# Kernel optimization log

Measured on AMD Instinct MI355X. Metric: run time of the kernel, lower is better.

Reference implementation:

```python
import jax, jax.numpy as jnp
import numpy as np

N_NODES = 100000
N_REL = 8
N_EDGES = 1_600_000
ED = 64   # entity_dim
RD = 64   # relation_dim
H = 4     # attention heads
A = 16    # attention dim per head
D1, D2 = 32, 16  # conv_dim_list


def _leaky(x):
    return jax.nn.leaky_relu(x, 0.01)  # nn.LeakyReLU default slope


def _l2norm(x):
    n = jnp.sqrt(jnp.sum(x * x, axis=1, keepdims=True))
    return x / jnp.maximum(n, 1e-12)  # F.normalize(p=2, dim=1)


def setup_inputs() -> dict:
    key = jax.random.key(0)
    ks = jax.random.split(key, 16)
    s = 0.1
    return dict(
        src=jax.random.randint(ks[0], (N_EDGES,), 0, N_NODES),
        dst=jax.random.randint(ks[1], (N_EDGES,), 0, N_NODES),
        etype=jax.random.randint(ks[2], (N_EDGES,), 0, N_REL),
        node_ids=jnp.arange(N_NODES),
        user_ids=jax.random.randint(ks[3], (1000,), 0, N_NODES),
        item_ids=jax.random.randint(ks[4], (4096,), 0, N_NODES),
        entity_embed=jax.random.normal(ks[5], (N_NODES, ED)) * s,
        rel_embed=jax.random.normal(ks[6], (N_REL, RD)) * s,
        W_R=jax.random.normal(ks[7], (N_REL, ED, RD)) * s,
        W_A=jax.random.normal(ks[8], (RD, H, A)) * s,
        W1_0=jax.random.normal(ks[9], (ED, D1 // H)) * s,
        b1_0=jnp.zeros((D1 // H,)),
        W2_0=jax.random.normal(ks[10], (ED, D1 // H)) * s,
        b2_0=jnp.zeros((D1 // H,)),
        W1_1=jax.random.normal(ks[11], (D1, D2 // H)) * s,
        b1_1=jnp.zeros((D2 // H,)),
        W2_1=jax.random.normal(ks[12], (D1, D2 // H)) * s,
        b2_1=jnp.zeros((D2 // H,)),
    )


def _compute_attention(entity_embed, rel_embed, W_R, W_A, src, dst, etype):
    # relation-specific edge attention: tanh(e_src W_r W_A) * tanh(e_dst W_r W_A + r W_A)
    WA_flat = W_A.reshape(RD, H * A)
    W_ra = jnp.einsum('rij,jk->rik', W_R, WA_flat)          # [R, ED, H*A]
    proj = jnp.einsum('ne,rek->rnk', entity_embed, W_ra)    # [R, N, H*A]
    r_emb_a = rel_embed @ WA_flat                           # [R, H*A]
    r_mul_t = jnp.tanh(proj[etype, src])                    # [E, H*A]
    r_mul_h = jnp.tanh(proj[etype, dst] + r_emb_a[etype])   # [E, H*A]
    att = (r_mul_t * r_mul_h).reshape(-1, H, A).sum(-1)     # [E, H]
    # edge softmax over incoming edges of each dst node, per head
    m = jax.ops.segment_max(att, dst, num_segments=N_NODES)
    m = jnp.where(jnp.isfinite(m), m, 0.0)
    e = jnp.exp(att - m[dst])
    z = jax.ops.segment_sum(e, dst, num_segments=N_NODES)
    return e / jnp.maximum(z[dst], 1e-12)                   # [E, H]


def _bi_layer(ego, att, src, dst, W1, b1, W2, b2, out_dim):
    # u_mul_e + sum: message = node[src] (broadcast over heads) * att[:, :, None]
    in_dim = ego.shape[1]
    msg = ego[src][:, None, :] * att[:, :, None]            # [E, H, in]
    N_h = jax.ops.segment_sum(msg, dst, num_segments=N_NODES)  # [N, H, in]
    node = ego[:, None, :]                                  # [N, 1, in]
    out1 = _leaky((node + N_h).reshape(-1, in_dim) @ W1 + b1).reshape(N_NODES, out_dim)
    out2 = _leaky((node * N_h).reshape(-1, in_dim) @ W2 + b2).reshape(N_NODES, out_dim)
    return out1 + out2  # dropout p=0 (eval)


def reference(src, dst, etype, node_ids, user_ids, item_ids,
              entity_embed, rel_embed, W_R, W_A,
              W1_0, b1_0, W2_0, b2_0, W1_1, b1_1, W2_1, b2_1):
    att = _compute_attention(entity_embed, rel_embed, W_R, W_A, src, dst, etype)
    ego = entity_embed[node_ids]
    ego1 = _bi_layer(ego, att, src, dst, W1_0, b1_0, W2_0, b2_0, D1)
    ego2 = _bi_layer(ego1, att, src, dst, W1_1, b1_1, W2_1, b2_1, D2)
    all_embed = jnp.concatenate([ego, _l2norm(ego1), _l2norm(ego2)], axis=1)  # [N, 112]
    return all_embed[user_ids] @ all_embed[item_ids].T     # [1000, 4096]
```

## Files before the change

### kernel.cpp

```cpp
#include <hip/hip_runtime.h>
#include <hip/hip_bf16.h>
#include <math.h>

#define NN 100000
#define NR 8
#define NE 1600000

typedef __attribute__((ext_vector_type(8))) short short8v;
typedef __attribute__((ext_vector_type(4))) float float4v;
typedef __attribute__((ext_vector_type(2))) float float2v;

__device__ inline float bf2f(unsigned short u) {
  union { unsigned int i; float f; } v; v.i = ((unsigned int)u) << 16; return v.f;
}
__device__ inline unsigned short f2bf(float f) {
  __hip_bfloat16 h = __float2bfloat16(f);
  return *reinterpret_cast<unsigned short*>(&h);
}
__device__ inline float fast_tanh(float x) {
  float ex = __expf(2.f * x);
  return 1.f - 2.f * __builtin_amdgcn_rcpf(ex + 1.f);
}

__global__ void k_prep(const float* __restrict__ W_R, const float* __restrict__ W_A,
                       const float* __restrict__ rel, unsigned short* __restrict__ Wbf,
                       float* __restrict__ r_emb_a) {
  int tid = blockIdx.x * 256 + threadIdx.x;
  if (tid < NR * 64 * 64) {
    int r = tid >> 12;
    int i = (tid >> 6) & 63;
    int k = tid & 63;
    float acc = 0.f;
    const float* wr = W_R + (r * 64 + i) * 64;
    for (int j = 0; j < 64; ++j) acc += wr[j] * W_A[j * 64 + k];
    Wbf[(r * 64 + k) * 64 + i] = f2bf(acc);
  } else if (tid < NR * 64 * 64 + NR * 64) {
    int idx = tid - NR * 64 * 64;
    int r = idx >> 6, k = idx & 63;
    float acc = 0.f;
    for (int j = 0; j < 64; ++j) acc += rel[r * 64 + j] * W_A[j * 64 + k];
    r_emb_a[idx] = acc;
  }
}

__global__ void k_cvt(const float* __restrict__ E, unsigned short* __restrict__ Ebf) {
  int i = blockIdx.x * 256 + threadIdx.x;
  float4 v = ((const float4*)E)[i];
  ushort4 o;
  o.x = f2bf(v.x); o.y = f2bf(v.y); o.z = f2bf(v.z); o.w = f2bf(v.w);
  ((ushort4*)Ebf)[i] = o;
}

__global__ void k_proj(const unsigned short* __restrict__ Ebf,
                       const unsigned short* __restrict__ Wbf,
                       const float* __restrict__ rea,
                       unsigned char* __restrict__ T1n, unsigned char* __restrict__ T2n) {
  int wv = threadIdx.x >> 6, lane = threadIdx.x & 63;
  int n0 = blockIdx.x * 64 + wv * 16;
  int mrow = lane & 15, kg = lane >> 4;
  int node = n0 + mrow;
  int nodeC = (node < NN) ? node : NN - 1;
  bool ok = (node < NN);
  const short8v b0 = *(const short8v*)(Ebf + (long)nodeC * 64 + kg * 8);
  const short8v b1 = *(const short8v*)(Ebf + (long)nodeC * 64 + 32 + kg * 8);
  for (int ct = 0; ct < 32; ++ct) {
    int ca = ct * 16 + mrow;
    const short8v a0 = *(const short8v*)(Wbf + ca * 64 + kg * 8);
    const short8v a1 = *(const short8v*)(Wbf + ca * 64 + 32 + kg * 8);
    float4v acc = {0.f, 0.f, 0.f, 0.f};
    acc = __builtin_amdgcn_mfma_f32_16x16x32_bf16(a0, b0, acc, 0, 0, 0);
    acc = __builtin_amdgcn_mfma_f32_16x16x32_bf16(a1, b1, acc, 0, 0, 0);
    int c0 = ct * 16 + kg * 4;
    float4 rv4 = *(const float4*)(rea + c0);
    unsigned int p1 = __builtin_amdgcn_cvt_pk_fp8_f32(fast_tanh(acc[0]), fast_tanh(acc[1]), 0u, false);
    p1 = __builtin_amdgcn_cvt_pk_fp8_f32(fast_tanh(acc[2]), fast_tanh(acc[3]), p1, true);
    unsigned int p2 = __builtin_amdgcn_cvt_pk_fp8_f32(fast_tanh(acc[0] + rv4.x), fast_tanh(acc[1] + rv4.y), 0u, false);
    p2 = __builtin_amdgcn_cvt_pk_fp8_f32(fast_tanh(acc[2] + rv4.z), fast_tanh(acc[3] + rv4.w), p2, true);
    if (ok) {
      *(unsigned int*)(T1n + (long)node * 512 + c0) = p1;
      *(unsigned int*)(T2n + (long)node * 512 + c0) = p2;
    }
  }
}

__global__ void k_hist(const int* __restrict__ dst, int* __restrict__ cnt) {
  int e = blockIdx.x * 256 + threadIdx.x;
  if (e < NE) atomicAdd(&cnt[dst[e]], 1);
}

#define SCAN_B 1024
#define NSCAN ((NN + SCAN_B - 1) / SCAN_B)

__global__ void k_scan1(const int* __restrict__ cnt, int* __restrict__ rowp,
                        int* __restrict__ bsum) {
  __shared__ int s[SCAN_B];
  int t = threadIdx.x, g = blockIdx.x * SCAN_B + t;
  s[t] = (g < NN) ? cnt[g] : 0;
  __syncthreads();
  for (int off = 1; off < SCAN_B; off <<= 1) {
    int x = (t >= off) ? s[t - off] : 0;
    __syncthreads();
    s[t] += x;
    __syncthreads();
  }
  if (g < NN) rowp[g + 1] = s[t];
  if (t == SCAN_B - 1) bsum[blockIdx.x] = s[t];
}

__global__ void k_scan2(int* bsum) {
  if (threadIdx.x == 0) {
    int acc = 0;
    for (int i = 0; i < NSCAN; ++i) { int v = bsum[i]; bsum[i] = acc; acc += v; }
  }
}

__global__ void k_scan3(int* rowp, const int* __restrict__ bsum) {
  int t = threadIdx.x, g = blockIdx.x * SCAN_B + t;
  if (g < NN) rowp[g + 1] += bsum[blockIdx.x];
  if (g == 0) rowp[0] = 0;
}

__global__ void k_scatter(const int* __restrict__ src, const int* __restrict__ dst,
                          const int* __restrict__ etype, const int* __restrict__ rowp,
                          int* __restrict__ cur, uint2* __restrict__ rec) {
  int e = blockIdx.x * 256 + threadIdx.x;
  if (e >= NE) return;
  int d = dst[e];
  int p = rowp[d] + atomicAdd(&cur[d], 1);
  uint2 rv;
  rv.x = ((unsigned int)src[e] << 3) | (unsigned int)etype[e];
  rv.y = (unsigned int)d;
  rec[p] = rv;
}

__global__ void k_att(const unsigned char* __restrict__ T1n,
                      const unsigned char* __restrict__ T2n,
                      const uint2* __restrict__ rec, int* __restrict__ srcs,
                      float* __restrict__ att) {
  int gid = blockIdx.x * 256 + threadIdx.x;
  int e = gid >> 2;
  int h = gid & 3;
  if (e >= NE) return;
  uint2 rv = rec[e];
  int r = rv.x & 7;
  int s = rv.x >> 3;
  int d = (int)rv.y;
  const uint4 av = *(const uint4*)(T1n + (long)s * 512 + r * 64 + h * 16);
  const uint4 bv = *(const uint4*)(T2n + (long)d * 512 + r * 64 + h * 16);
  const unsigned int* ap = (const unsigned int*)&av;
  const unsigned int* bp = (const unsigned int*)&bv;
  float acc = 0.f;
#pragma unroll
  for (int i = 0; i < 4; ++i) {
    float2v a0 = __builtin_amdgcn_cvt_pk_f32_fp8(ap[i], false);
    float2v a1 = __builtin_amdgcn_cvt_pk_f32_fp8(ap[i], true);
    float2v b0 = __builtin_amdgcn_cvt_pk_f32_fp8(bp[i], false);
    float2v b1 = __builtin_amdgcn_cvt_pk_f32_fp8(bp[i], true);
    acc += a0.x * b0.x + a0.y * b0.y + a1.x * b1.x + a1.y * b1.y;
  }
  att[gid] = acc;
  if (h == 0) srcs[e] = s;
}

__global__ void k_nodemax(const int* __restrict__ rowp, const float* __restrict__ att,
                          float* __restrict__ minv) {
  int gid = blockIdx.x * 256 + threadIdx.x;
  int n = gid >> 2, h = gid & 3;
  if (n >= NN) return;
  int p0 = rowp[n], p1 = rowp[n + 1];
  float m = -3.4e38f;
  for (int p = p0; p < p1; ++p) m = fmaxf(m, att[p * 4 + h]);
  float z = 0.f;
  for (int p = p0; p < p1; ++p) z += __expf(att[p * 4 + h] - m);
  minv[n * 8 + h] = m;
  minv[n * 8 + 4 + h] = 1.f / fmaxf(z, 1e-12f);
}

__global__ void k_fused0(const float* __restrict__ E, const unsigned short* __restrict__ Ebf,
                         const float* __restrict__ att, const float* __restrict__ minv,
                         const int* __restrict__ rowp, const int* __restrict__ srcs,
                         const float* __restrict__ W1, const float* __restrict__ b1,
                         const float* __restrict__ W2, const float* __restrict__ b2,
                         float* __restrict__ ego1, unsigned short* __restrict__ ego1bf) {
  __shared__ float wt1[8][68], wt2[8][68];
  __shared__ float bb[16];
  __shared__ float s1[4][4][68], s2[4][4][68];
  int t = threadIdx.x;
  for (int i = t; i < 512; i += 256) {
    int d = i >> 3, j = i & 7;
    wt1[j][d] = W1[i];
    wt2[j][d] = W2[i];
  }
  if (t < 8) bb[t] = b1[t];
  else if (t < 16) bb[t] = b2[t - 8];
  __syncthreads();
  int wv = t >> 6, lane = t & 63;
  int n = blockIdx.x * 4 + wv;
  int p0 = rowp[n], p1 = rowp[n + 1];
  int g = lane >> 4, q = lane & 15;
  float4 mh = *(const float4*)(minv + n * 8);
  float4 zh = *(const float4*)(minv + n * 8 + 4);
  float acc[4][4];
#pragma unroll
  for (int h = 0; h < 4; ++h)
#pragma unroll
    for (int j = 0; j < 4; ++j) acc[h][j] = 0.f;
  for (int p = p0 + g; p < p1; p += 4) {
    int s = srcs[p];
    float4 a = ((const float4*)att)[p];
    a.x = __expf(a.x - mh.x) * zh.x;
    a.y = __expf(a.y - mh.y) * zh.y;
    a.z = __expf(a.z - mh.z) * zh.z;
    a.w = __expf(a.w - mh.w) * zh.w;
    ushort4 ev = *(const ushort4*)(Ebf + s * 64 + q * 4);
    float e0 = bf2f(ev.x), e1 = bf2f(ev.y), e2 = bf2f(ev.z), e3 = bf2f(ev.w);
    acc[0][0] += a.x * e0; acc[0][1] += a.x * e1; acc[0][2] += a.x * e2; acc[0][3] += a.x * e3;
    acc[1][0] += a.y * e0; acc[1][1] += a.y * e1; acc[1][2] += a.y * e2; acc[1][3] += a.y * e3;
    acc[2][0] += a.z * e0; acc[2][1] += a.z * e1; acc[2][2] += a.z * e2; acc[2][3] += a.z * e3;
    acc[3][0] += a.w * e0; acc[3][1] += a.w * e1; acc[3][2] += a.w * e2; acc[3][3] += a.w * e3;
  }
#pragma unroll
  for (int h = 0; h < 4; ++h)
#pragma unroll
    for (int j = 0; j < 4; ++j) {
      acc[h][j] += __shfl_xor(acc[h][j], 16);
      acc[h][j] += __shfl_xor(acc[h][j], 32);
    }
  if (lane < 16) {
    float4 edv = *(const float4*)(E + n * 64 + q * 4);
#pragma unroll
    for (int h = 0; h < 4; ++h) {
      float4 v1, v2;
      v1.x = edv.x + acc[h][0]; v2.x = edv.x * acc[h][0];
      v1.y = edv.y + acc[h][1]; v2.y = edv.y * acc[h][1];
      v1.z = edv.z + acc[h][2]; v2.z = edv.z * acc[h][2];
      v1.w = edv.w + acc[h][3]; v2.w = edv.w * acc[h][3];
      *(float4*)&s1[wv][h][q * 4] = v1;
      *(float4*)&s2[wv][h][q * 4] = v2;
    }
  }
  __syncthreads();
  int h = (lane >> 3) & 3, j = lane & 7;
  const float* sp = (lane < 32) ? &s1[wv][h][0] : &s2[wv][h][0];
  const float* wp = (lane < 32) ? &wt1[j][0] : &wt2[j][0];
  float o = 0.f;
#pragma unroll
  for (int d = 0; d < 64; d += 4) {
    float4 sv = *(const float4*)(sp + d);
    float4 wv4 = *(const float4*)(wp + d);
    o += sv.x * wv4.x + sv.y * wv4.y + sv.z * wv4.z + sv.w * wv4.w;
  }
  o += (lane < 32) ? bb[j] : bb[8 + j];
  o = (o >= 0.f) ? o : 0.01f * o;
  float other = __shfl_xor(o, 32);
  if (lane < 32) {
    float r = o + other;
    ego1[n * 32 + h * 8 + j] = r;
    ego1bf[n * 32 + h * 8 + j] = f2bf(r);
  }
}

__global__ void k_fused1(const float* __restrict__ ego1, const unsigned short* __restrict__ E1bf,
                         const float* __restrict__ att, const float* __restrict__ minv,
                         const int* __restrict__ rowp, const int* __restrict__ srcs,
                         const float* __restrict__ W1, const float* __restrict__ b1,
                         const float* __restrict__ W2, const float* __restrict__ b2,
                         float* __restrict__ ego2) {
  __shared__ float wt1[4][36], wt2[4][36], bb[8];
  __shared__ float s1[4][4][36], s2[4][4][36];
  int t = threadIdx.x;
  if (t < 128) { int d = t >> 2, j = t & 3; wt1[j][d] = W1[t]; wt2[j][d] = W2[t]; }
  if (t < 4) bb[t] = b1[t];
  else if (t < 8) bb[t] = b2[t - 4];
  __syncthreads();
  int wv = t >> 6, lane = t & 63;
  int n = blockIdx.x * 4 + wv;
  int p0 = rowp[n], p1 = rowp[n + 1];
  int g = lane >> 3, q = lane & 7;
  float4 mh = *(const float4*)(minv + n * 8);
  float4 zh = *(const float4*)(minv + n * 8 + 4);
  float acc[4][4];
#pragma unroll
  for (int h = 0; h < 4; ++h)
#pragma unroll
    for (int j = 0; j < 4; ++j) acc[h][j] = 0.f;
  for (int p = p0 + g; p < p1; p += 8) {
    int s = srcs[p];
    float4 a = ((const float4*)att)[p];
    a.x = __expf(a.x - mh.x) * zh.x;
    a.y = __expf(a.y - mh.y) * zh.y;
    a.z = __expf(a.z - mh.z) * zh.z;
    a.w = __expf(a.w - mh.w) * zh.w;
    ushort4 ev = *(const ushort4*)(E1bf + s * 32 + q * 4);
    float e0 = bf2f(ev.x), e1 = bf2f(ev.y), e2 = bf2f(ev.z), e3 = bf2f(ev.w);
    acc[0][0] += a.x * e0; acc[0][1] += a.x * e1; acc[0][2] += a.x * e2; acc[0][3] += a.x * e3;
    acc[1][0] += a.y * e0; acc[1][1] += a.y * e1; acc[1][2] += a.y * e2; acc[1][3] += a.y * e3;
    acc[2][0] += a.z * e0; acc[2][1] += a.z * e1; acc[2][2] += a.z * e2; acc[2][3] += a.z * e3;
    acc[3][0] += a.w * e0; acc[3][1] += a.w * e1; acc[3][2] += a.w * e2; acc[3][3] += a.w * e3;
  }
#pragma unroll
  for (int h = 0; h < 4; ++h)
#pragma unroll
    for (int j = 0; j < 4; ++j) {
      acc[h][j] += __shfl_xor(acc[h][j], 8);
      acc[h][j] += __shfl_xor(acc[h][j], 16);
      acc[h][j] += __shfl_xor(acc[h][j], 32);
    }
  if (lane < 8) {
    float4 e1v = *(const float4*)(ego1 + n * 32 + q * 4);
#pragma unroll
    for (int h = 0; h < 4; ++h) {
      float4 v1, v2;
      v1.x = e1v.x + acc[h][0]; v2.x = e1v.x * acc[h][0];
      v1.y = e1v.y + acc[h][1]; v2.y = e1v.y * acc[h][1];
      v1.z = e1v.z + acc[h][2]; v2.z = e1v.z * acc[h][2];
      v1.w = e1v.w + acc[h][3]; v2.w = e1v.w * acc[h][3];
      *(float4*)&s1[wv][h][q * 4] = v1;
      *(float4*)&s2[wv][h][q * 4] = v2;
    }
  }
  __syncthreads();
  if (lane < 32) {
    int h = (lane >> 2) & 3, j = lane & 3;
    const float* sp = (lane < 16) ? &s1[wv][h][0] : &s2[wv][h][0];
    const float* wp = (lane < 16) ? &wt1[j][0] : &wt2[j][0];
    float o = 0.f;
#pragma unroll
    for (int d = 0; d < 32; d += 4) {
      float4 sv = *(const float4*)(sp + d);
      float4 wv4 = *(const float4*)(wp + d);
      o += sv.x * wv4.x + sv.y * wv4.y + sv.z * wv4.z + sv.w * wv4.w;
    }
    o += (lane < 16) ? bb[j] : bb[4 + j];
    o = (o >= 0.f) ? o : 0.01f * o;
    float other = __shfl_xor(o, 16);
    if (lane < 16) ego2[n * 16 + h * 4 + j] = o + other;
  }
}

__global__ void k_uv(const float* __restrict__ E, const float* __restrict__ E1,
                     const float* __restrict__ E2, const int* __restrict__ uid,
                     const int* __restrict__ iid, float* __restrict__ U,
                     float* __restrict__ V) {
  int row = (blockIdx.x * 256 + threadIdx.x) >> 6;
  int lane = threadIdx.x & 63;
  if (row >= 1000 + 4096) return;
  int id = (row < 1000) ? uid[row] : iid[row - 1000];
  float* dest = (row < 1000) ? (U + row * 112) : (V + (row - 1000) * 112);
  float v1 = (lane < 32) ? E1[id * 32 + lane] : 0.f;
  float s1 = v1 * v1;
  for (int m = 1; m < 64; m <<= 1) s1 += __shfl_xor(s1, m);
  float v2 = (lane < 16) ? E2[id * 16 + lane] : 0.f;
  float s2 = v2 * v2;
  for (int m = 1; m < 64; m <<= 1) s2 += __shfl_xor(s2, m);
  float i1 = 1.f / fmaxf(sqrtf(s1), 1e-12f);
  float i2 = 1.f / fmaxf(sqrtf(s2), 1e-12f);
  dest[lane] = E[id * 64 + lane];
  if (lane < 32) dest[64 + lane] = v1 * i1;
  if (lane < 16) dest[96 + lane] = v2 * i2;
}

__global__ void k_gemm(const float* __restrict__ U, const float* __restrict__ V,
                       float* __restrict__ C) {
  __shared__ float Us[16][113], Vs[16][113];
  int tx = threadIdx.x & 15, ty = threadIdx.x >> 4;
  int u0 = blockIdx.y * 16, v0 = blockIdx.x * 16;
  for (int i = threadIdx.x; i < 16 * 112; i += 256) {
    int rr = i / 112, cc = i % 112;
    int ur = u0 + rr;
    Us[rr][cc] = (ur < 1000) ? U[ur * 112 + cc] : 0.f;
    Vs[rr][cc] = V[(v0 + rr) * 112 + cc];
  }
  __syncthreads();
  int u = u0 + ty;
  if (u >= 1000) return;
  float acc = 0.f;
#pragma unroll
  for (int k = 0; k < 112; ++k) acc += Us[ty][k] * Vs[tx][k];
  C[u * 4096 + v0 + tx] = acc;
}

extern "C" void kernel_launch(void* const* d_in, const int* in_sizes, int n_in,
                              void* d_out, int out_size, void* d_ws, size_t ws_size,
                              hipStream_t stream) {
  const int* src = (const int*)d_in[0];
  const int* dst = (const int*)d_in[1];
  const int* etype = (const int*)d_in[2];
  const int* uid = (const int*)d_in[4];
  const int* iid = (const int*)d_in[5];
  const float* entity = (const float*)d_in[6];
  const float* rel = (const float*)d_in[7];
  const float* W_R = (const float*)d_in[8];
  const float* W_A = (const float*)d_in[9];
  const float* W1_0 = (const float*)d_in[10];
  const float* b1_0 = (const float*)d_in[11];
  const float* W2_0 = (const float*)d_in[12];
  const float* b2_0 = (const float*)d_in[13];
  const float* W1_1 = (const float*)d_in[14];
  const float* b1_1 = (const float*)d_in[15];
  const float* W2_1 = (const float*)d_in[16];
  const float* b2_1 = (const float*)d_in[17];
  float* out = (float*)d_out;

  char* ws = (char*)d_ws;
  unsigned char*  T1n  = (unsigned char*) (ws + 0);
  float*          ego1 = (float*)         (ws + 0);
  unsigned short* e1bf = (unsigned short*)(ws + 12800000);
  float*          ego2 = (float*)         (ws + 19200000);
  float*          U    = (float*)         (ws + 25600000);
  float*          V    = (float*)         (ws + 26048000);
  unsigned char*  T2n  = (unsigned char*) (ws + 51200000);
  float*          att  = (float*)         (ws + 102400000);
  uint2*          rec  = (uint2*)         (ws + 128000000);
  int*            srcs = (int*)           (ws + 140800000);
  int*            rowp = (int*)           (ws + 147200000);
  int*            cnt  = (int*)           (ws + 147600128);
  int*            bsum = (int*)           (ws + 148000256);
  unsigned short* Wbf  = (unsigned short*)(ws + 148000768);
  float*          rea  = (float*)         (ws + 148066304);
  unsigned short* Ebf  = (unsigned short*)(ws + 148068352);
  float*          minv = (float*)         (ws + 160868352);

  hipMemsetAsync(cnt, 0, NN * sizeof(int), stream);
  k_prep<<<130, 256, 0, stream>>>(W_R, W_A, rel, Wbf, rea);
  k_cvt<<<6250, 256, 0, stream>>>(entity, Ebf);
  k_proj<<<(NN + 63) / 64, 256, 0, stream>>>(Ebf, Wbf, rea, T1n, T2n);
  k_hist<<<NE / 256, 256, 0, stream>>>(dst, cnt);
  k_scan1<<<NSCAN, SCAN_B, 0, stream>>>(cnt, rowp, bsum);
  k_scan2<<<1, 64, 0, stream>>>(bsum);
  k_scan3<<<NSCAN, SCAN_B, 0, stream>>>(rowp, bsum);
  hipMemsetAsync(cnt, 0, NN * sizeof(int), stream);
  k_scatter<<<NE / 256, 256, 0, stream>>>(src, dst, etype, rowp, cnt, rec);
  k_att<<<NE * 4 / 256, 256, 0, stream>>>(T1n, T2n, rec, srcs, att);
  k_nodemax<<<(NN * 4 + 255) / 256, 256, 0, stream>>>(rowp, att, minv);
  k_fused0<<<NN / 4, 256, 0, stream>>>(entity, Ebf, att, minv, rowp, srcs,
                                       W1_0, b1_0, W2_0, b2_0, ego1, e1bf);
  k_fused1<<<NN / 4, 256, 0, stream>>>(ego1, e1bf, att, minv, rowp, srcs,
                                       W1_1, b1_1, W2_1, b2_1, ego2);
  k_uv<<<(1000 + 4096 + 3) / 4, 256, 0, stream>>>(entity, ego1, ego2, uid, iid, U, V);
  k_gemm<<<dim3(4096 / 16, (1000 + 15) / 16), 256, 0, stream>>>(U, V, out);
}
```

Baseline: 594.8 us.

## Fuse edge attention and softmax normalization into layer-0 aggregation kernel

Computes edge attention dot products inside the per-destination-node aggregation kernel, drops the separate attention and segment-max/sum kernels, and skips the max subtraction since attention values are bounded. Unnormalized exp weights are accumulated and the sum reciprocal is applied at the end; exp weights and inverse sums are stored for the second layer. This removes two launches and the round trips for att, srcs and min/inv stats, at the cost of extra shuffles per edge inside the fused loop and reliance on bounded logits for numerical safety.

```diff
diff --git a/kernel.cpp b/kernel.cpp
--- a/kernel.cpp
+++ b/kernel.cpp
@@ -133,52 +133,11 @@
   rec[p] = rv;
 }
 
-__global__ void k_att(const unsigned char* __restrict__ T1n,
-                      const unsigned char* __restrict__ T2n,
-                      const uint2* __restrict__ rec, int* __restrict__ srcs,
-                      float* __restrict__ att) {
-  int gid = blockIdx.x * 256 + threadIdx.x;
-  int e = gid >> 2;
-  int h = gid & 3;
-  if (e >= NE) return;
-  uint2 rv = rec[e];
-  int r = rv.x & 7;
-  int s = rv.x >> 3;
-  int d = (int)rv.y;
-  const uint4 av = *(const uint4*)(T1n + (long)s * 512 + r * 64 + h * 16);
-  const uint4 bv = *(const uint4*)(T2n + (long)d * 512 + r * 64 + h * 16);
-  const unsigned int* ap = (const unsigned int*)&av;
-  const unsigned int* bp = (const unsigned int*)&bv;
-  float acc = 0.f;
-#pragma unroll
-  for (int i = 0; i < 4; ++i) {
-    float2v a0 = __builtin_amdgcn_cvt_pk_f32_fp8(ap[i], false);
-    float2v a1 = __builtin_amdgcn_cvt_pk_f32_fp8(ap[i], true);
-    float2v b0 = __builtin_amdgcn_cvt_pk_f32_fp8(bp[i], false);
-    float2v b1 = __builtin_amdgcn_cvt_pk_f32_fp8(bp[i], true);
-    acc += a0.x * b0.x + a0.y * b0.y + a1.x * b1.x + a1.y * b1.y;
-  }
-  att[gid] = acc;
-  if (h == 0) srcs[e] = s;
-}
-
-__global__ void k_nodemax(const int* __restrict__ rowp, const float* __restrict__ att,
-                          float* __restrict__ minv) {
-  int gid = blockIdx.x * 256 + threadIdx.x;
-  int n = gid >> 2, h = gid & 3;
-  if (n >= NN) return;
-  int p0 = rowp[n], p1 = rowp[n + 1];
-  float m = -3.4e38f;
-  for (int p = p0; p < p1; ++p) m = fmaxf(m, att[p * 4 + h]);
-  float z = 0.f;
-  for (int p = p0; p < p1; ++p) z += __expf(att[p * 4 + h] - m);
-  minv[n * 8 + h] = m;
-  minv[n * 8 + 4 + h] = 1.f / fmaxf(z, 1e-12f);
-}
-
 __global__ void k_fused0(const float* __restrict__ E, const unsigned short* __restrict__ Ebf,
-                         const float* __restrict__ att, const float* __restrict__ minv,
-                         const int* __restrict__ rowp, const int* __restrict__ srcs,
+                         const unsigned char* __restrict__ T1n,
+                         const unsigned char* __restrict__ T2n,
+                         const uint2* __restrict__ rec, const int* __restrict__ rowp,
+                         float* __restrict__ att4, float* __restrict__ zinv4,
                          const float* __restrict__ W1, const float* __restrict__ b1,
                          const float* __restrict__ W2, const float* __restrict__ b2,
                          float* __restrict__ ego1, unsigned short* __restrict__ ego1bf) {
@@ -198,26 +157,39 @@
   int n = blockIdx.x * 4 + wv;
   int p0 = rowp[n], p1 = rowp[n + 1];
   int g = lane >> 4, q = lane & 15;
-  float4 mh = *(const float4*)(minv + n * 8);
-  float4 zh = *(const float4*)(minv + n * 8 + 4);
+  int bl = (lane & 48) | (lane & 3);
+  const unsigned int* recw = (const unsigned int*)rec;
   float acc[4][4];
 #pragma unroll
   for (int h = 0; h < 4; ++h)
 #pragma unroll
     for (int j = 0; j < 4; ++j) acc[h][j] = 0.f;
+  float z0 = 0.f, z1 = 0.f, z2 = 0.f, z3 = 0.f;
   for (int p = p0 + g; p < p1; p += 4) {
-    int s = srcs[p];
-    float4 a = ((const float4*)att)[p];
-    a.x = __expf(a.x - mh.x) * zh.x;
-    a.y = __expf(a.y - mh.y) * zh.y;
-    a.z = __expf(a.z - mh.z) * zh.z;
-    a.w = __expf(a.w - mh.w) * zh.w;
+    unsigned int rv = recw[p * 2];
+    int s = (int)(rv >> 3), r = (int)(rv & 7);
+    unsigned int aw = *(const unsigned int*)(T1n + (long)s * 512 + r * 64 + q * 4);
+    unsigned int bw = *(const unsigned int*)(T2n + (long)n * 512 + r * 64 + q * 4);
+    float2v fa0 = __builtin_amdgcn_cvt_pk_f32_fp8(aw, false);
+    float2v fa1 = __builtin_amdgcn_cvt_pk_f32_fp8(aw, true);
+    float2v fb0 = __builtin_amdgcn_cvt_pk_f32_fp8(bw, false);
+    float2v fb1 = __builtin_amdgcn_cvt_pk_f32_fp8(bw, true);
+    float dot = fa0.x * fb0.x + fa0.y * fb0.y + fa1.x * fb1.x + fa1.y * fb1.y;
+    dot += __shfl_xor(dot, 1);
+    dot += __shfl_xor(dot, 2);
+    float e = __expf(dot);
+    float e0 = __shfl(e, bl);
+    float e1 = __shfl(e, bl + 4);
+    float e2 = __shfl(e, bl + 8);
+    float e3 = __shfl(e, bl + 12);
+    z0 += e0; z1 += e1; z2 += e2; z3 += e3;
+    if (q == 0) ((float4*)att4)[p] = make_float4(e0, e1, e2, e3);
     ushort4 ev = *(const ushort4*)(Ebf + s * 64 + q * 4);
-    float e0 = bf2f(ev.x), e1 = bf2f(ev.y), e2 = bf2f(ev.z), e3 = bf2f(ev.w);
-    acc[0][0] += a.x * e0; acc[0][1] += a.x * e1; acc[0][2] += a.x * e2; acc[0][3] += a.x * e3;
-    acc[1][0] += a.y * e0; acc[1][1] += a.y * e1; acc[1][2] += a.y * e2; acc[1][3] += a.y * e3;
-    acc[2][0] += a.z * e0; acc[2][1] += a.z * e1; acc[2][2] += a.z * e2; acc[2][3] += a.z * e3;
-    acc[3][0] += a.w * e0; acc[3][1] += a.w * e1; acc[3][2] += a.w * e2; acc[3][3] += a.w * e3;
+    float v0 = bf2f(ev.x), v1 = bf2f(ev.y), v2 = bf2f(ev.z), v3 = bf2f(ev.w);
+    acc[0][0] += e0 * v0; acc[0][1] += e0 * v1; acc[0][2] += e0 * v2; acc[0][3] += e0 * v3;
+    acc[1][0] += e1 * v0; acc[1][1] += e1 * v1; acc[1][2] += e1 * v2; acc[1][3] += e1 * v3;
+    acc[2][0] += e2 * v0; acc[2][1] += e2 * v1; acc[2][2] += e2 * v2; acc[2][3] += e2 * v3;
+    acc[3][0] += e3 * v0; acc[3][1] += e3 * v1; acc[3][2] += e3 * v2; acc[3][3] += e3 * v3;
   }
 #pragma unroll
   for (int h = 0; h < 4; ++h)
@@ -226,17 +198,30 @@
       acc[h][j] += __shfl_xor(acc[h][j], 16);
       acc[h][j] += __shfl_xor(acc[h][j], 32);
     }
+  z0 += __shfl_xor(z0, 16); z0 += __shfl_xor(z0, 32);
+  z1 += __shfl_xor(z1, 16); z1 += __shfl_xor(z1, 32);
+  z2 += __shfl_xor(z2, 16); z2 += __shfl_xor(z2, 32);
+  z3 += __shfl_xor(z3, 16); z3 += __shfl_xor(z3, 32);
+  float zi0 = 1.f / fmaxf(z0, 1e-12f);
+  float zi1 = 1.f / fmaxf(z1, 1e-12f);
+  float zi2 = 1.f / fmaxf(z2, 1e-12f);
+  float zi3 = 1.f / fmaxf(z3, 1e-12f);
+  if (lane == 0) *(float4*)(zinv4 + n * 4) = make_float4(zi0, zi1, zi2, zi3);
   if (lane < 16) {
+    acc[0][0] *= zi0; acc[0][1] *= zi0; acc[0][2] *= zi0; acc[0][3] *= zi0;
+    acc[1][0] *= zi1; acc[1][1] *= zi1; acc[1][2] *= zi1; acc[1][3] *= zi1;
+    acc[2][0] *= zi2; acc[2][1] *= zi2; acc[2][2] *= zi2; acc[2][3] *= zi2;
+    acc[3][0] *= zi3; acc[3][1] *= zi3; acc[3][2] *= zi3; acc[3][3] *= zi3;
     float4 edv = *(const float4*)(E + n * 64 + q * 4);
 #pragma unroll
     for (int h = 0; h < 4; ++h) {
-      float4 v1, v2;
-      v1.x = edv.x + acc[h][0]; v2.x = edv.x * acc[h][0];
-      v1.y = edv.y + acc[h][1]; v2.y = edv.y * acc[h][1];
-      v1.z = edv.z + acc[h][2]; v2.z = edv.z * acc[h][2];
-      v1.w = edv.w + acc[h][3]; v2.w = edv.w * acc[h][3];
-      *(float4*)&s1[wv][h][q * 4] = v1;
-      *(float4*)&s2[wv][h][q * 4] = v2;
+      float4 v1v, v2v;
+      v1v.x = edv.x + acc[h][0]; v2v.x = edv.x * acc[h][0];
+      v1v.y = edv.y + acc[h][1]; v2v.y = edv.y * acc[h][1];
+      v1v.z = edv.z + acc[h][2]; v2v.z = edv.z * acc[h][2];
+      v1v.w = edv.w + acc[h][3]; v2v.w = edv.w * acc[h][3];
+      *(float4*)&s1[wv][h][q * 4] = v1v;
+      *(float4*)&s2[wv][h][q * 4] = v2v;
     }
   }
   __syncthreads();
@@ -261,8 +246,8 @@
 }
 
 __global__ void k_fused1(const float* __restrict__ ego1, const unsigned short* __restrict__ E1bf,
-                         const float* __restrict__ att, const float* __restrict__ minv,
-                         const int* __restrict__ rowp, const int* __restrict__ srcs,
+                         const float* __restrict__ att4, const float* __restrict__ zinv4,
+                         const uint2* __restrict__ rec, const int* __restrict__ rowp,
                          const float* __restrict__ W1, const float* __restrict__ b1,
                          const float* __restrict__ W2, const float* __restrict__ b2,
                          float* __restrict__ ego2) {
@@ -277,20 +262,15 @@
   int n = blockIdx.x * 4 + wv;
   int p0 = rowp[n], p1 = rowp[n + 1];
   int g = lane >> 3, q = lane & 7;
-  float4 mh = *(const float4*)(minv + n * 8);
-  float4 zh = *(const float4*)(minv + n * 8 + 4);
+  const unsigned int* recw = (const unsigned int*)rec;
   float acc[4][4];
 #pragma unroll
   for (int h = 0; h < 4; ++h)
 #pragma unroll
     for (int j = 0; j < 4; ++j) acc[h][j] = 0.f;
   for (int p = p0 + g; p < p1; p += 8) {
-    int s = srcs[p];
-    float4 a = ((const float4*)att)[p];
-    a.x = __expf(a.x - mh.x) * zh.x;
-    a.y = __expf(a.y - mh.y) * zh.y;
-    a.z = __expf(a.z - mh.z) * zh.z;
-    a.w = __expf(a.w - mh.w) * zh.w;
+    int s = (int)(recw[p * 2] >> 3);
+    float4 a = ((const float4*)att4)[p];
     ushort4 ev = *(const ushort4*)(E1bf + s * 32 + q * 4);
     float e0 = bf2f(ev.x), e1 = bf2f(ev.y), e2 = bf2f(ev.z), e3 = bf2f(ev.w);
     acc[0][0] += a.x * e0; acc[0][1] += a.x * e1; acc[0][2] += a.x * e2; acc[0][3] += a.x * e3;
@@ -307,6 +287,11 @@
       acc[h][j] += __shfl_xor(acc[h][j], 32);
     }
   if (lane < 8) {
+    float4 zi = *(const float4*)(zinv4 + n * 4);
+#pragma unroll
+    for (int j = 0; j < 4; ++j) {
+      acc[0][j] *= zi.x; acc[1][j] *= zi.y; acc[2][j] *= zi.z; acc[3][j] *= zi.w;
+    }
     float4 e1v = *(const float4*)(ego1 + n * 32 + q * 4);
 #pragma unroll
     for (int h = 0; h < 4; ++h) {
@@ -326,9 +311,9 @@
     const float* wp = (lane < 16) ? &wt1[j][0] : &wt2[j][0];
     float o = 0.f;
 #pragma unroll
-    for (int d = 0; d < 32; d += 4) {
-      float4 sv = *(const float4*)(sp + d);
-      float4 wv4 = *(const float4*)(wp + d);
+    for (int dd = 0; dd < 32; dd += 4) {
+      float4 sv = *(const float4*)(sp + dd);
+      float4 wv4 = *(const float4*)(wp + dd);
       o += sv.x * wv4.x + sv.y * wv4.y + sv.z * wv4.z + sv.w * wv4.w;
     }
     o += (lane < 16) ? bb[j] : bb[4 + j];
@@ -404,22 +389,21 @@
 
   char* ws = (char*)d_ws;
   unsigned char*  T1n  = (unsigned char*) (ws + 0);
-  float*          ego1 = (float*)         (ws + 0);
-  unsigned short* e1bf = (unsigned short*)(ws + 12800000);
-  float*          ego2 = (float*)         (ws + 19200000);
-  float*          U    = (float*)         (ws + 25600000);
-  float*          V    = (float*)         (ws + 26048000);
   unsigned char*  T2n  = (unsigned char*) (ws + 51200000);
-  float*          att  = (float*)         (ws + 102400000);
+  float*          att4 = (float*)         (ws + 102400000);
   uint2*          rec  = (uint2*)         (ws + 128000000);
-  int*            srcs = (int*)           (ws + 140800000);
-  int*            rowp = (int*)           (ws + 147200000);
-  int*            cnt  = (int*)           (ws + 147600128);
-  int*            bsum = (int*)           (ws + 148000256);
-  unsigned short* Wbf  = (unsigned short*)(ws + 148000768);
-  float*          rea  = (float*)         (ws + 148066304);
-  unsigned short* Ebf  = (unsigned short*)(ws + 148068352);
-  float*          minv = (float*)         (ws + 160868352);
+  int*            rowp = (int*)           (ws + 140800000);
+  int*            cnt  = (int*)           (ws + 141200128);
+  int*            bsum = (int*)           (ws + 141600256);
+  unsigned short* Wbf  = (unsigned short*)(ws + 141600768);
+  float*          rea  = (float*)         (ws + 141666304);
+  unsigned short* Ebf  = (unsigned short*)(ws + 141668352);
+  float*          zinv4= (float*)         (ws + 154468352);
+  float*          ego1 = (float*)         (ws + 156068352);
+  unsigned short* e1bf = (unsigned short*)(ws + 168868352);
+  float*          ego2 = (float*)         (ws + 175268352);
+  float*          U    = (float*)         (ws + 181668352);
+  float*          V    = (float*)         (ws + 182116352);
 
   hipMemsetAsync(cnt, 0, NN * sizeof(int), stream);
   k_prep<<<130, 256, 0, stream>>>(W_R, W_A, rel, Wbf, rea);
@@ -431,11 +415,10 @@
   k_scan3<<<NSCAN, SCAN_B, 0, stream>>>(rowp, bsum);
   hipMemsetAsync(cnt, 0, NN * sizeof(int), stream);
   k_scatter<<<NE / 256, 256, 0, stream>>>(src, dst, etype, rowp, cnt, rec);
-  k_att<<<NE * 4 / 256, 256, 0, stream>>>(T1n, T2n, rec, srcs, att);
-  k_nodemax<<<(NN * 4 + 255) / 256, 256, 0, stream>>>(rowp, att, minv);
-  k_fused0<<<NN / 4, 256, 0, stream>>>(entity, Ebf, att, minv, rowp, srcs,
-                                       W1_0, b1_0, W2_0, b2_0, ego1, e1bf);
-  k_fused1<<<NN / 4, 256, 0, stream>>>(ego1, e1bf, att, minv, rowp, srcs,
+  k_fused0<<<NN / 4, 256, 0, stream>>>(entity, Ebf, T1n, T2n, rec, rowp,
+                                       att4, zinv4, W1_0, b1_0, W2_0, b2_0,
+                                       ego1, e1bf);
+  k_fused1<<<NN / 4, 256, 0, stream>>>(ego1, e1bf, att4, zinv4, rec, rowp,
                                        W1_1, b1_1, W2_1, b2_1, ego2);
   k_uv<<<(1000 + 4096 + 3) / 4, 256, 0, stream>>>(entity, ego1, ego2, uid, iid, U, V);
   k_gemm<<<dim3(4096 / 16, (1000 + 15) / 16), 256, 0, stream>>>(U, V, out);
```

After: 581.4 us. 1.02x faster.
